# Performance work log

Measured on AMD Instinct MI355X. Metric: run time of the kernel, lower is better.

## Reference

```python
import jax, jax.numpy as jnp
import numpy as np

N, E, D, H, G = 100000, 1600000, 128, 256, 64
N0, N1 = 50000, 25000
SLOPE = 0.01  # PyTorch LeakyReLU default


def lrelu(x):
    return jax.nn.leaky_relu(x, SLOPE)


def seg_sum(x, idx, n):
    return jax.ops.segment_sum(x, idx, num_segments=n)


def seg_max(x, idx, n):
    m = jax.ops.segment_max(x, idx, num_segments=n)
    return jnp.where(jnp.isneginf(m), jnp.zeros_like(m), m)


def mpnn(x, edge_index, edge_attr, w1, b1, g, be, w2, b2):
    # MPNN.forward: add_self_loops -> node MLP -> sym-normalized, edge-weighted scatter-add
    n = x.shape[0]
    ar = jnp.arange(n)
    row = jnp.concatenate([edge_index[0], ar])  # source j (x_j gathered here)
    col = jnp.concatenate([edge_index[1], ar])  # target i (aggregation index)
    ea = jnp.concatenate([edge_attr, jnp.ones((n,), x.dtype)])  # self-loop fill=1.0
    # Linear -> BatchNorm1d(eval: mean0/var1) -> Dropout(eval: id) -> LeakyReLU -> Linear
    h = lrelu((x @ w1.T + b1) * g + be) @ w2.T + b2
    deg = seg_sum(jnp.ones(row.shape, x.dtype), row, n)
    dis = jnp.where(deg > 0, deg ** -0.5, 0.0)
    norm = dis[row] * dis[col]
    msg = (norm * ea)[:, None] * h[row]  # gather + elementwise weighting
    return seg_sum(msg, col, n)          # scatter-add aggregation


def _forward(x, edge_attr, energy, params, edge_index, batch, cluster0, cluster1):
    (w0a, b0a, g0, be0, w0b, b0b,
     w1a, b1a, g1, be1, w1b, b1b,
     w2a, b2a, g2, be2, w2b, b2b,
     emb_w, emb_b, emb_g, emb_be,
     lw1, lb1, lg, lbe, lw2, lb2) = params
    h = mpnn(x, edge_index, edge_attr, w0a, b0a, g0, be0, w0b, b0b) + x
    # --- first graclus max_pool (cluster0 precomputed; edges mapped w/o coalesce) ---
    px = seg_max(lrelu(h), cluster0, N0)
    ox = seg_max(x, cluster0, N0)  # max_pool(origin)
    pe = cluster0[edge_index]
    pb = jnp.maximum(jax.ops.segment_max(batch, cluster0, num_segments=N0), 0)
    # NOTE: mpnn_1 output is assigned to a local `x` and discarded in the original forward,
    # so it does not affect the result; we skip the dead computation.
    h2 = px + ox
    # --- second graclus max_pool ---
    px2 = seg_max(lrelu(h2), cluster1, N1)
    pe2 = cluster1[pe]
    pb2 = jnp.maximum(jax.ops.segment_max(pb, cluster1, num_segments=N1), 0)
    h3 = lrelu(mpnn(px2, pe2, edge_attr, w2a, b2a, g2, be2, w2b, b2b))
    gx = seg_max(h3, pb2, G)  # global_max_pool
    e = lrelu((energy.reshape(G, 21) @ emb_w.T + emb_b) * emb_g + emb_be)
    z = jnp.concatenate([gx, e], axis=1)  # [G, D+8]
    z = lrelu((z @ lw1.T + lb1) * lg + lbe)
    return z @ lw2.T + lb2  # [G, 1]


def setup_inputs() -> dict:
    key = jax.random.key(0)
    ks = iter(jax.random.split(key, 40))

    def lin(k, fo, fi):  # kaiming_normal_ fan_in, leaky_relu
        return jax.random.normal(k, (fo, fi), jnp.float32) * np.float32(np.sqrt(2.0 / fi))

    def bias(n):
        return jnp.full((n,), 0.01, jnp.float32)

    inp = {}
    inp['x'] = jax.random.normal(next(ks), (N, D), jnp.float32)
    inp['edge_attr'] = jax.random.uniform(next(ks), (E,), jnp.float32)
    inp['energy'] = jax.random.normal(next(ks), (G * 21,), jnp.float32)
    # mpnn_0 (D->D->D)
    inp['w0a'] = lin(next(ks), D, D); inp['b0a'] = bias(D)
    inp['g0'] = jnp.ones((D,), jnp.float32); inp['be0'] = jnp.zeros((D,), jnp.float32)
    inp['w0b'] = lin(next(ks), D, D); inp['b0b'] = bias(D)
    # mpnn_1 (D->D->D)  (dead in forward, kept as params)
    inp['w1a'] = lin(next(ks), D, D); inp['b1a'] = bias(D)
    inp['g1'] = jnp.ones((D,), jnp.float32); inp['be1'] = jnp.zeros((D,), jnp.float32)
    inp['w1b'] = lin(next(ks), D, D); inp['b1b'] = bias(D)
    # mpnn_2 (D->H->D)
    inp['w2a'] = lin(next(ks), H, D); inp['b2a'] = bias(H)
    inp['g2'] = jnp.ones((H,), jnp.float32); inp['be2'] = jnp.zeros((H,), jnp.float32)
    inp['w2b'] = lin(next(ks), D, H); inp['b2b'] = bias(D)
    # emb (21->8)
    inp['emb_w'] = lin(next(ks), 8, 21); inp['emb_b'] = bias(8)
    inp['emb_g'] = jnp.ones((8,), jnp.float32); inp['emb_be'] = jnp.zeros((8,), jnp.float32)
    # head ((D+8)->D->1)
    inp['lw1'] = lin(next(ks), D, D + 8); inp['lb1'] = bias(D)
    inp['lg'] = jnp.ones((D,), jnp.float32); inp['lbe'] = jnp.zeros((D,), jnp.float32)
    inp['lw2'] = lin(next(ks), 1, D); inp['lb2'] = bias(1)
    # int inputs
    inp['edge_index'] = jax.random.randint(next(ks), (2, E), 0, N, dtype=jnp.int32)
    inp['batch'] = jnp.sort(jax.random.randint(next(ks), (N,), 0, G, dtype=jnp.int32))
    inp['cluster0'] = jax.random.randint(next(ks), (N,), 0, N0, dtype=jnp.int32)
    inp['cluster1'] = jax.random.randint(next(ks), (N0,), 0, N1, dtype=jnp.int32)
    return inp


def reference(x, edge_attr, energy,
              w0a, b0a, g0, be0, w0b, b0b,
              w1a, b1a, g1, be1, w1b, b1b,
              w2a, b2a, g2, be2, w2b, b2b,
              emb_w, emb_b, emb_g, emb_be,
              lw1, lb1, lg, lbe, lw2, lb2,
              edge_index, batch, cluster0, cluster1):
    params = (w0a, b0a, g0, be0, w0b, b0b,
              w1a, b1a, g1, be1, w1b, b1b,
              w2a, b2a, g2, be2, w2b, b2b,
              emb_w, emb_b, emb_g, emb_be,
              lw1, lb1, lg, lbe, lw2, lb2)
    return _forward(x, edge_attr, energy, params, edge_index, batch, cluster0, cluster1)
```

## Files before the change

kernel.cpp:

```cpp
#include <hip/hip_runtime.h>
#include <math.h>

#define N_NODES 100000
#define N_EDGES 1600000
#define DIM     128
#define NPOOL0  50000
#define NPOOL1  25000
#define NGRAPH  64

typedef __attribute__((ext_vector_type(8))) short short8;
typedef __attribute__((ext_vector_type(4))) float f32x4;

__device__ __forceinline__ float lrelu(float v) { return v > 0.f ? v : 0.01f * v; }

__device__ __forceinline__ unsigned short f2bf(float f) {
    unsigned u = __float_as_uint(f);
    unsigned r = u + 0x7FFFu + ((u >> 16) & 1u);
    return (unsigned short)(r >> 16);
}

__device__ __forceinline__ void atomicMaxF(float* addr, float val) {
    if (val >= 0.f) atomicMax((int*)addr, __float_as_int(val));
    else            atomicMin((unsigned int*)addr, __float_as_uint(val));
}

__global__ __launch_bounds__(256) void fill_f32(float* __restrict__ p, int n, float v) {
    int i = blockIdx.x * 256 + threadIdx.x;
    if (i < n) p[i] = v;
}
__global__ __launch_bounds__(256) void fill_i32(int* __restrict__ p, int n, int v) {
    int i = blockIdx.x * 256 + threadIdx.x;
    if (i < n) p[i] = v;
}
__global__ __launch_bounds__(256) void conv_bf16(const float* __restrict__ in, unsigned short* __restrict__ out, int n) {
    int i = blockIdx.x * 256 + threadIdx.x;
    if (i < n) out[i] = f2bf(in[i]);
}

template<int KIN, int HID, bool BF16IN>
__global__ __launch_bounds__(256) void mlp_mfma(
        const void* __restrict__ Xv, int R,
        const unsigned short* __restrict__ W1, const float* __restrict__ B1,
        const float* __restrict__ G1, const float* __restrict__ BE1,
        const unsigned short* __restrict__ W2, const float* __restrict__ B2,
        unsigned short* __restrict__ Y)
{
    constexpr int XS_S = KIN + 8;
    constexpr int TS_S = HID + 8;
    __shared__ unsigned short xs[64 * XS_S];
    __shared__ unsigned short ts[64 * TS_S];

    const int tid = threadIdx.x;
    const int r0 = blockIdx.x * 64;

    {
        const int row = tid >> 2;
        const int c0 = (tid & 3) * 32;
        const int gr = r0 + row;
        if (BF16IN) {
            const unsigned short* X = (const unsigned short*)Xv;
            #pragma unroll
            for (int q = 0; q < 4; ++q) {
                short8 v = short8{0,0,0,0,0,0,0,0};
                if (gr < R) v = *(const short8*)&X[(size_t)gr * KIN + c0 + q * 8];
                *(short8*)&xs[row * XS_S + c0 + q * 8] = v;
            }
        } else {
            const float* X = (const float*)Xv;
            #pragma unroll
            for (int q = 0; q < 4; ++q) {
                short8 v = short8{0,0,0,0,0,0,0,0};
                if (gr < R) {
                    float4 a = *(const float4*)&X[(size_t)gr * KIN + c0 + q * 8];
                    float4 b = *(const float4*)&X[(size_t)gr * KIN + c0 + q * 8 + 4];
                    v[0] = (short)f2bf(a.x); v[1] = (short)f2bf(a.y);
                    v[2] = (short)f2bf(a.z); v[3] = (short)f2bf(a.w);
                    v[4] = (short)f2bf(b.x); v[5] = (short)f2bf(b.y);
                    v[6] = (short)f2bf(b.z); v[7] = (short)f2bf(b.w);
                }
                *(short8*)&xs[row * XS_S + c0 + q * 8] = v;
            }
        }
    }
    __syncthreads();

    const int wv = tid >> 6;
    const int lane = tid & 63;
    const int lr = lane & 15;
    const int lq = lane >> 4;
    const int arow = wv * 16 + lr;

    constexpr int NCG1 = HID / 16;
    constexpr int NK1 = KIN / 32;
    f32x4 acc1[NCG1] = {};
    for (int kc = 0; kc < NK1; ++kc) {
        short8 a = *(short8*)&xs[arow * XS_S + kc * 32 + lq * 8];
        #pragma unroll
        for (int cg = 0; cg < NCG1; ++cg) {
            short8 b = *(const short8*)&W1[(size_t)(cg * 16 + lr) * KIN + kc * 32 + lq * 8];
            acc1[cg] = __builtin_amdgcn_mfma_f32_16x16x32_bf16(a, b, acc1[cg], 0, 0, 0);
        }
    }
    #pragma unroll
    for (int cg = 0; cg < NCG1; ++cg) {
        const int c = cg * 16 + lr;
        const float bb = B1[c], gg = G1[c], ee = BE1[c];
        #pragma unroll
        for (int q = 0; q < 4; ++q) {
            const int rr = wv * 16 + lq * 4 + q;
            float v = (acc1[cg][q] + bb) * gg + ee;
            ts[rr * TS_S + c] = f2bf(lrelu(v));
        }
    }

    constexpr int NK2 = HID / 32;
    f32x4 acc2[8] = {};
    for (int kc = 0; kc < NK2; ++kc) {
        short8 a = *(short8*)&ts[arow * TS_S + kc * 32 + lq * 8];
        #pragma unroll
        for (int cg = 0; cg < 8; ++cg) {
            short8 b = *(const short8*)&W2[(size_t)(cg * 16 + lr) * HID + kc * 32 + lq * 8];
            acc2[cg] = __builtin_amdgcn_mfma_f32_16x16x32_bf16(a, b, acc2[cg], 0, 0, 0);
        }
    }
    #pragma unroll
    for (int cg = 0; cg < 8; ++cg) {
        const int c = cg * 16 + lr;
        const float bb = B2[c];
        #pragma unroll
        for (int q = 0; q < 4; ++q) {
            const int gr = r0 + wv * 16 + lq * 4 + q;
            if (gr < R) Y[(size_t)gr * 128 + c] = f2bf(acc2[cg][q] + bb);
        }
    }
}

__global__ __launch_bounds__(256) void count0(const int* __restrict__ src, const int* __restrict__ dst,
                                              float* __restrict__ deg, int* __restrict__ cnt, int E) {
    int e = blockIdx.x * 256 + threadIdx.x;
    if (e < E) {
        atomicAdd(&deg[src[e]], 1.0f);
        atomicAdd(&cnt[dst[e]], 1);
    }
}
__global__ __launch_bounds__(256) void rsqrt_ip(float* __restrict__ p, int n) {
    int i = blockIdx.x * 256 + threadIdx.x;
    if (i < n) p[i] = rsqrtf(p[i]);
}
__global__ __launch_bounds__(256) void scan_blk(const int* __restrict__ cnt, int* __restrict__ offs,
                                                int* __restrict__ bsum, int n) {
    __shared__ int s[256];
    const int tid = threadIdx.x;
    const int i = blockIdx.x * 256 + tid;
    int v = (i < n) ? cnt[i] : 0;
    s[tid] = v;
    __syncthreads();
    #pragma unroll
    for (int d = 1; d < 256; d <<= 1) {
        int t = (tid >= d) ? s[tid - d] : 0;
        __syncthreads();
        s[tid] += t;
        __syncthreads();
    }
    if (i < n) offs[i] = s[tid] - v;
    if (tid == 255) bsum[blockIdx.x] = s[255];
}
__global__ __launch_bounds__(512) void scan_top(int* __restrict__ bsum, int nb) {
    __shared__ int s[512];
    const int tid = threadIdx.x;
    int v = (tid < nb) ? bsum[tid] : 0;
    s[tid] = v;
    __syncthreads();
    #pragma unroll
    for (int d = 1; d < 512; d <<= 1) {
        int t = (tid >= d) ? s[tid - d] : 0;
        __syncthreads();
        s[tid] += t;
        __syncthreads();
    }
    if (tid < nb) bsum[tid] = s[tid] - v;
}
__global__ __launch_bounds__(256) void scan_add(int* __restrict__ offs, const int* __restrict__ bsum,
                                                int* __restrict__ fill, int n) {
    int i = blockIdx.x * 256 + threadIdx.x;
    if (i < n) {
        int o = offs[i] + bsum[i >> 8];
        offs[i] = o;
        fill[i] = o;
    }
}
__global__ __launch_bounds__(256) void place_pack(const int* __restrict__ dst, const int* __restrict__ srcA,
                                                  const float* __restrict__ ea, const float* __restrict__ dis,
                                                  int* __restrict__ fill, int2* __restrict__ pack, int E) {
    int e = blockIdx.x * 256 + threadIdx.x;
    if (e < E) {
        int d = dst[e];
        int s = srcA[e];
        int pos = atomicAdd(&fill[d], 1);
        pack[pos] = make_int2(s, __float_as_int(dis[s] * ea[e]));
    }
}
__global__ __launch_bounds__(256) void edgemap(
        const int* __restrict__ ei0, const int* __restrict__ ei1,
        const int* __restrict__ c0, const int* __restrict__ c1,
        int* __restrict__ src2, int* __restrict__ dst2,
        float* __restrict__ deg2, int* __restrict__ cnt2, int E)
{
    int e = blockIdx.x * 256 + threadIdx.x;
    if (e < E) {
        int s = c1[c0[ei0[e]]];
        int d = c1[c0[ei1[e]]];
        src2[e] = s;
        dst2[e] = d;
        atomicAdd(&deg2[s], 1.0f);
        atomicAdd(&cnt2[d], 1);
    }
}
__global__ __launch_bounds__(256) void seg_count(const int* __restrict__ map, int* __restrict__ cnt, int n) {
    int i = blockIdx.x * 256 + threadIdx.x;
    if (i < n) atomicAdd(&cnt[map[i]], 1);
}
__global__ __launch_bounds__(256) void place_idx(const int* __restrict__ map, int* __restrict__ fill,
                                                 int* __restrict__ list, int n) {
    int i = blockIdx.x * 256 + threadIdx.x;
    if (i < n) {
        int pos = atomicAdd(&fill[map[i]], 1);
        list[pos] = i;
    }
}
__global__ __launch_bounds__(256) void segmax_i32(const int* __restrict__ map, const int* __restrict__ vals,
                                                  int* __restrict__ out, int n) {
    int i = blockIdx.x * 256 + threadIdx.x;
    if (i < n) atomicMax(&out[map[i]], vals[i]);
}

#define EDGE_ITER(K, A0, A1) {                                                  \
    int s_ = __builtin_amdgcn_readlane(pv.x, (K));                              \
    float w_ = __int_as_float(__builtin_amdgcn_readlane(pv.y, (K)));            \
    unsigned hv_ = hrows[(size_t)s_ * 64 + lane];                               \
    float c_ = w_ * di;                                                         \
    A0 += c_ * __uint_as_float(hv_ << 16);                                      \
    A1 += c_ * __uint_as_float(hv_ & 0xFFFF0000u); }

__global__ __launch_bounds__(256) void gather0(
        const unsigned short* __restrict__ h16, const float* __restrict__ x,
        const float* __restrict__ dis, const int* __restrict__ offs,
        const int* __restrict__ cnt, const int2* __restrict__ pack,
        unsigned* __restrict__ agg0)
{
    const int wid = (blockIdx.x * 256 + threadIdx.x) >> 6;
    if (wid >= N_NODES) return;
    const int lane = threadIdx.x & 63;
    const float di = dis[wid];
    const unsigned* hrows = (const unsigned*)h16;

    unsigned hself = hrows[(size_t)wid * 64 + lane];
    float a0 = di * di * __uint_as_float(hself << 16);
    float a1 = di * di * __uint_as_float(hself & 0xFFFF0000u);
    float b0 = 0.f, b1 = 0.f;

    const int base = offs[wid], n = cnt[wid];
    int k0 = 0;
    for (; k0 + 64 <= n; k0 += 64) {
        int2 pv = pack[base + k0 + lane];
        #pragma unroll
        for (int k = 0; k < 64; k += 2) {
            EDGE_ITER(k,     a0, a1);
            EDGE_ITER(k + 1, b0, b1);
        }
    }
    const int rem = n - k0;
    if (rem > 0) {
        int2 pv = (lane < rem) ? pack[base + k0 + lane] : make_int2(0, 0);
        #pragma unroll 4
        for (int k = 0; k < rem; ++k) EDGE_ITER(k, a0, a1);
    }
    a0 += b0; a1 += b1;

    float2 xv = *(const float2*)&x[(size_t)wid * DIM + lane * 2];
    agg0[(size_t)wid * 64 + lane] =
        ((unsigned)f2bf(a1 + xv.y) << 16) | (unsigned)f2bf(a0 + xv.x);
}

__global__ __launch_bounds__(256) void gather2(
        const unsigned short* __restrict__ hm2,
        const float* __restrict__ dis, const int* __restrict__ offs,
        const int* __restrict__ cnt, const int2* __restrict__ pack,
        float* __restrict__ agg2)
{
    const int wid = (blockIdx.x * 256 + threadIdx.x) >> 6;
    if (wid >= NPOOL1) return;
    const int lane = threadIdx.x & 63;
    const float di = dis[wid];
    const unsigned* hrows = (const unsigned*)hm2;

    unsigned hself = hrows[(size_t)wid * 64 + lane];
    float a0 = di * di * __uint_as_float(hself << 16);
    float a1 = di * di * __uint_as_float(hself & 0xFFFF0000u);
    float b0 = 0.f, b1 = 0.f;

    const int base = offs[wid], n = cnt[wid];
    int k0 = 0;
    for (; k0 + 64 <= n; k0 += 64) {
        int2 pv = pack[base + k0 + lane];
        #pragma unroll
        for (int k = 0; k < 64; k += 2) {
            EDGE_ITER(k,     a0, a1);
            EDGE_ITER(k + 1, b0, b1);
        }
    }
    const int rem = n - k0;
    if (rem > 0) {
        int2 pv = (lane < rem) ? pack[base + k0 + lane] : make_int2(0, 0);
        #pragma unroll 4
        for (int k = 0; k < rem; ++k) EDGE_ITER(k, a0, a1);
    }
    a0 += b0; a1 += b1;

    float2 o = make_float2(lrelu(a0), lrelu(a1));
    *(float2*)&agg2[(size_t)wid * DIM + lane * 2] = o;
}

__global__ __launch_bounds__(256) void pool1_gather(
        const unsigned* __restrict__ agg0, const float* __restrict__ x,
        const int* __restrict__ offsc, const int* __restrict__ cntc,
        const int* __restrict__ listc, unsigned* __restrict__ h2)
{
    const int c = (blockIdx.x * 256 + threadIdx.x) >> 6;
    if (c >= NPOOL0) return;
    const int lane = threadIdx.x & 63;
    const int base = offsc[c], n = cntc[c];
    float p0 = -INFINITY, p1 = -INFINITY, o0 = -INFINITY, o1 = -INFINITY;
    for (int k = 0; k < n; ++k) {
        const int node = listc[base + k];
        const unsigned hv = agg0[(size_t)node * 64 + lane];
        const float2 xv = *(const float2*)&x[(size_t)node * 128 + lane * 2];
        p0 = fmaxf(p0, lrelu(__uint_as_float(hv << 16)));
        p1 = fmaxf(p1, lrelu(__uint_as_float(hv & 0xFFFF0000u)));
        o0 = fmaxf(o0, xv.x);
        o1 = fmaxf(o1, xv.y);
    }
    p0 = (p0 == -INFINITY) ? 0.f : p0;
    p1 = (p1 == -INFINITY) ? 0.f : p1;
    o0 = (o0 == -INFINITY) ? 0.f : o0;
    o1 = (o1 == -INFINITY) ? 0.f : o1;
    h2[(size_t)c * 64 + lane] =
        ((unsigned)f2bf(p1 + o1) << 16) | (unsigned)f2bf(p0 + o0);
}

__global__ __launch_bounds__(256) void pool2_gather(
        const unsigned* __restrict__ h2,
        const int* __restrict__ offsd, const int* __restrict__ cntd,
        const int* __restrict__ listd, unsigned* __restrict__ x2)
{
    const int d = (blockIdx.x * 256 + threadIdx.x) >> 6;
    if (d >= NPOOL1) return;
    const int lane = threadIdx.x & 63;
    const int base = offsd[d], n = cntd[d];
    float m0 = -INFINITY, m1 = -INFINITY;
    for (int k = 0; k < n; ++k) {
        const int node = listd[base + k];
        const unsigned hv = h2[(size_t)node * 64 + lane];
        m0 = fmaxf(m0, lrelu(__uint_as_float(hv << 16)));
        m1 = fmaxf(m1, lrelu(__uint_as_float(hv & 0xFFFF0000u)));
    }
    m0 = (m0 == -INFINITY) ? 0.f : m0;
    m1 = (m1 == -INFINITY) ? 0.f : m1;
    x2[(size_t)d * 64 + lane] = ((unsigned)f2bf(m1) << 16) | (unsigned)f2bf(m0);
}

__global__ __launch_bounds__(256) void gpool_scan(
        const float* __restrict__ agg2, const int* __restrict__ listg,
        const int* __restrict__ pb2, float* __restrict__ gmax)
{
    const int wave = (blockIdx.x * 256 + threadIdx.x) >> 6;
    const int lane = threadIdx.x & 63;
    const int CH = (NPOOL1 + 511) / 512;
    const int p0 = wave * CH;
    const int p1 = min(p0 + CH, NPOOL1);
    if (p0 >= NPOOL1) return;

    float m0 = -INFINITY, m1 = -INFINITY;
    int cur = -1;
    for (int p = p0; p < p1; ++p) {
        const int node = listg[p];
        const int g = pb2[node];
        if (g != cur) {
            if (cur >= 0) {
                float* gp = &gmax[(size_t)cur * DIM + lane * 2];
                atomicMaxF(gp + 0, m0);
                atomicMaxF(gp + 1, m1);
            }
            cur = g; m0 = -INFINITY; m1 = -INFINITY;
        }
        const float2 v = *(const float2*)&agg2[(size_t)node * DIM + lane * 2];
        m0 = fmaxf(m0, v.x);
        m1 = fmaxf(m1, v.y);
    }
    float* gp = &gmax[(size_t)cur * DIM + lane * 2];
    atomicMaxF(gp + 0, m0);
    atomicMaxF(gp + 1, m1);
}

__global__ __launch_bounds__(128) void head(
        const float* __restrict__ gmax, const float* __restrict__ energy,
        const float* __restrict__ emb_w, const float* __restrict__ emb_b,
        const float* __restrict__ emb_g, const float* __restrict__ emb_be,
        const float* __restrict__ lw1, const float* __restrict__ lb1,
        const float* __restrict__ lg, const float* __restrict__ lbe,
        const float* __restrict__ lw2, const float* __restrict__ lb2,
        float* __restrict__ out)
{
    const int g = blockIdx.x;
    const int t = threadIdx.x;
    __shared__ float z[136];
    __shared__ float red[128];

    {
        float v = gmax[(size_t)g * DIM + t];
        z[t] = (v == -INFINITY) ? 0.f : v;
    }
    if (t < 8) {
        float s = 0.f;
        #pragma unroll
        for (int k = 0; k < 21; ++k) s += energy[g * 21 + k] * emb_w[t * 21 + k];
        s = (s + emb_b[t]) * emb_g[t] + emb_be[t];
        z[128 + t] = lrelu(s);
    }
    __syncthreads();
    float s = 0.f;
    #pragma unroll 8
    for (int k = 0; k < 136; ++k) s += z[k] * lw1[t * 136 + k];
    float z2 = lrelu((s + lb1[t]) * lg[t] + lbe[t]);
    red[t] = z2 * lw2[t];
    __syncthreads();
    if (t == 0) {
        float acc = lb2[0];
        for (int k = 0; k < 128; ++k) acc += red[k];
        out[g] = acc;
    }
}

extern "C" void kernel_launch(void* const* d_in, const int* in_sizes, int n_in,
                              void* d_out, int out_size, void* d_ws, size_t ws_size,
                              hipStream_t stream) {
    const float* x        = (const float*)d_in[0];
    const float* edge_attr= (const float*)d_in[1];
    const float* energy   = (const float*)d_in[2];
    const float* w0a = (const float*)d_in[3];
    const float* b0a = (const float*)d_in[4];
    const float* g0  = (const float*)d_in[5];
    const float* be0 = (const float*)d_in[6];
    const float* w0b = (const float*)d_in[7];
    const float* b0b = (const float*)d_in[8];
    const float* w2a = (const float*)d_in[15];
    const float* b2a = (const float*)d_in[16];
    const float* g2  = (const float*)d_in[17];
    const float* be2 = (const float*)d_in[18];
    const float* w2b = (const float*)d_in[19];
    const float* b2b = (const float*)d_in[20];
    const float* emb_w  = (const float*)d_in[21];
    const float* emb_b  = (const float*)d_in[22];
    const float* emb_g  = (const float*)d_in[23];
    const float* emb_be = (const float*)d_in[24];
    const float* lw1 = (const float*)d_in[25];
    const float* lb1 = (const float*)d_in[26];
    const float* lg  = (const float*)d_in[27];
    const float* lbe = (const float*)d_in[28];
    const float* lw2 = (const float*)d_in[29];
    const float* lb2 = (const float*)d_in[30];
    const int* ei0   = (const int*)d_in[31];
    const int* ei1   = ei0 + N_EDGES;
    const int* batch = (const int*)d_in[32];
    const int* c0    = (const int*)d_in[33];
    const int* c1    = (const int*)d_in[34];
    float* out = (float*)d_out;

    char* ws = (char*)d_ws;
    unsigned short* h16 = (unsigned short*)(ws + 0);
    int*   src2  = (int*)(ws + 0);
    int*   dst2  = (int*)(ws + 6400000);
    float* agg2  = (float*)(ws + 12800000);
    unsigned* agg0 = (unsigned*)(ws + 25600000);
    unsigned short* hm2 = (unsigned short*)(ws + 25600000);
    int2*  pack0 = (int2*)(ws + 51200000);
    int2*  pack2 = (int2*)(ws + 51200000);
    unsigned* h2 = (unsigned*)(ws + 64000000);
    unsigned* x2 = (unsigned*)(ws + 76800000);
    float* deg0  = (float*)(ws + 83200000);
    int*   cnt0  = (int*)(ws + 83600000);
    int*   offs0 = (int*)(ws + 84000000);
    int*   fill0 = (int*)(ws + 84400000);
    int*   cntc  = (int*)(ws + 84800000);
    int*   offsc = (int*)(ws + 85000000);
    int*   fillc = (int*)(ws + 85200000);
    int*   listc = (int*)(ws + 85400000);
    int*   pb    = (int*)(ws + 85800000);
    int*   pb2   = (int*)(ws + 86000000);
    int*   cntd  = (int*)(ws + 86100000);
    int*   offsd = (int*)(ws + 86200000);
    int*   filld = (int*)(ws + 86300000);
    int*   listd = (int*)(ws + 86400000);
    float* deg2  = (float*)(ws + 86600000);
    int*   cnt2  = (int*)(ws + 86700000);
    int*   offs2 = (int*)(ws + 86800000);
    int*   fill2 = (int*)(ws + 86900000);
    int*   cntg  = (int*)(ws + 87000000);
    int*   offsg = (int*)(ws + 87000256);
    int*   fillg = (int*)(ws + 87000512);
    int*   listg = (int*)(ws + 87001088);
    int*   bsum  = (int*)(ws + 87102096);
    unsigned short* w0a16 = (unsigned short*)(ws + 87105000);
    unsigned short* w0b16 = (unsigned short*)(ws + 87138000);
    unsigned short* w2a16 = (unsigned short*)(ws + 87171000);
    unsigned short* w2b16 = (unsigned short*)(ws + 87237000);
    float* gmax  = (float*)(ws + 87303000);

    (void)in_sizes; (void)n_in; (void)out_size; (void)ws_size;

    const int NB0 = (N_NODES + 255) / 256;
    const int NBC = (NPOOL0 + 255) / 256;
    const int NB1 = (NPOOL1 + 255) / 256;
    const int NBE = (N_EDGES + 255) / 256;

    conv_bf16<<<64, 256, 0, stream>>>(w0a, w0a16, 16384);
    conv_bf16<<<64, 256, 0, stream>>>(w0b, w0b16, 16384);
    conv_bf16<<<128, 256, 0, stream>>>(w2a, w2a16, 32768);
    conv_bf16<<<128, 256, 0, stream>>>(w2b, w2b16, 32768);

    fill_f32<<<NB0, 256, 0, stream>>>(deg0, N_NODES, 1.0f);
    fill_i32<<<NB0, 256, 0, stream>>>(cnt0, N_NODES, 0);
    mlp_mfma<128, 128, false><<<(N_NODES + 63) / 64, 256, 0, stream>>>(
        x, N_NODES, w0a16, b0a, g0, be0, w0b16, b0b, h16);
    count0<<<NBE, 256, 0, stream>>>(ei0, ei1, deg0, cnt0, N_EDGES);
    rsqrt_ip<<<NB0, 256, 0, stream>>>(deg0, N_NODES);
    scan_blk<<<NB0, 256, 0, stream>>>(cnt0, offs0, bsum, N_NODES);
    scan_top<<<1, 512, 0, stream>>>(bsum, NB0);
    scan_add<<<NB0, 256, 0, stream>>>(offs0, bsum, fill0, N_NODES);
    place_pack<<<NBE, 256, 0, stream>>>(ei1, ei0, edge_attr, deg0, fill0, pack0, N_EDGES);
    gather0<<<(N_NODES * 64) / 256, 256, 0, stream>>>(h16, x, deg0, offs0, cnt0, pack0, agg0);

    fill_i32<<<NBC, 256, 0, stream>>>(cntc, NPOOL0, 0);
    seg_count<<<NB0, 256, 0, stream>>>(c0, cntc, N_NODES);
    scan_blk<<<NBC, 256, 0, stream>>>(cntc, offsc, bsum, NPOOL0);
    scan_top<<<1, 512, 0, stream>>>(bsum, NBC);
    scan_add<<<NBC, 256, 0, stream>>>(offsc, bsum, fillc, NPOOL0);
    place_idx<<<NB0, 256, 0, stream>>>(c0, fillc, listc, N_NODES);
    fill_i32<<<NBC, 256, 0, stream>>>(pb, NPOOL0, 0);
    segmax_i32<<<NB0, 256, 0, stream>>>(c0, batch, pb, N_NODES);
    pool1_gather<<<(NPOOL0 * 64) / 256, 256, 0, stream>>>(agg0, x, offsc, cntc, listc, h2);

    fill_i32<<<NB1, 256, 0, stream>>>(cntd, NPOOL1, 0);
    seg_count<<<NBC, 256, 0, stream>>>(c1, cntd, NPOOL0);
    scan_blk<<<NB1, 256, 0, stream>>>(cntd, offsd, bsum, NPOOL1);
    scan_top<<<1, 512, 0, stream>>>(bsum, NB1);
    scan_add<<<NB1, 256, 0, stream>>>(offsd, bsum, filld, NPOOL1);
    place_idx<<<NBC, 256, 0, stream>>>(c1, filld, listd, NPOOL0);
    fill_i32<<<NB1, 256, 0, stream>>>(pb2, NPOOL1, 0);
    segmax_i32<<<NBC, 256, 0, stream>>>(c1, pb, pb2, NPOOL0);
    pool2_gather<<<(NPOOL1 * 64) / 256, 256, 0, stream>>>(h2, offsd, cntd, listd, x2);

    fill_f32<<<NB1, 256, 0, stream>>>(deg2, NPOOL1, 1.0f);
    fill_i32<<<NB1, 256, 0, stream>>>(cnt2, NPOOL1, 0);
    edgemap<<<NBE, 256, 0, stream>>>(ei0, ei1, c0, c1, src2, dst2, deg2, cnt2, N_EDGES);
    rsqrt_ip<<<NB1, 256, 0, stream>>>(deg2, NPOOL1);
    scan_blk<<<NB1, 256, 0, stream>>>(cnt2, offs2, bsum, NPOOL1);
    scan_top<<<1, 512, 0, stream>>>(bsum, NB1);
    scan_add<<<NB1, 256, 0, stream>>>(offs2, bsum, fill2, NPOOL1);
    mlp_mfma<128, 256, true><<<(NPOOL1 + 63) / 64, 256, 0, stream>>>(
        x2, NPOOL1, w2a16, b2a, g2, be2, w2b16, b2b, hm2);
    place_pack<<<NBE, 256, 0, stream>>>(dst2, src2, edge_attr, deg2, fill2, pack2, N_EDGES);
    gather2<<<(NPOOL1 * 64) / 256, 256, 0, stream>>>(hm2, deg2, offs2, cnt2, pack2, agg2);

    fill_i32<<<1, 256, 0, stream>>>(cntg, NGRAPH, 0);
    seg_count<<<NB1, 256, 0, stream>>>(pb2, cntg, NPOOL1);
    scan_blk<<<1, 256, 0, stream>>>(cntg, offsg, bsum, NGRAPH);
    scan_top<<<1, 512, 0, stream>>>(bsum, 1);
    scan_add<<<1, 256, 0, stream>>>(offsg, bsum, fillg, NGRAPH);
    place_idx<<<NB1, 256, 0, stream>>>(pb2, fillg, listg, NPOOL1);
    fill_f32<<<(NGRAPH * DIM + 255) / 256, 256, 0, stream>>>(gmax, NGRAPH * DIM, -INFINITY);
    gpool_scan<<<128, 256, 0, stream>>>(agg2, listg, pb2, gmax);
    head<<<NGRAPH, 128, 0, stream>>>(gmax, energy, emb_w, emb_b, emb_g, emb_be,
                                     lw1, lb1, lg, lbe, lw2, lb2, out);
}
```

Baseline: 1.219 ms.

## Derive pooled-graph degrees from node degrees and batch init kernels

```diff
diff --git a/kernel.cpp b/kernel.cpp
--- a/kernel.cpp
+++ b/kernel.cpp
@@ -24,17 +24,23 @@
     else            atomicMin((unsigned int*)addr, __float_as_uint(val));
 }
 
-__global__ __launch_bounds__(256) void fill_f32(float* __restrict__ p, int n, float v) {
-    int i = blockIdx.x * 256 + threadIdx.x;
-    if (i < n) p[i] = v;
-}
-__global__ __launch_bounds__(256) void fill_i32(int* __restrict__ p, int n, int v) {
-    int i = blockIdx.x * 256 + threadIdx.x;
-    if (i < n) p[i] = v;
-}
-__global__ __launch_bounds__(256) void conv_bf16(const float* __restrict__ in, unsigned short* __restrict__ out, int n) {
-    int i = blockIdx.x * 256 + threadIdx.x;
-    if (i < n) out[i] = f2bf(in[i]);
+__global__ __launch_bounds__(256) void init_f(float* __restrict__ deg0, float* __restrict__ deg2,
+                                              float* __restrict__ gmax) {
+    int i = blockIdx.x * 256 + threadIdx.x;
+    if (i < N_NODES) deg0[i] = 1.0f;
+    else if (i < N_NODES + NPOOL1) deg2[i - N_NODES] = 1.0f;
+    else if (i < N_NODES + NPOOL1 + NGRAPH * DIM) gmax[i - N_NODES - NPOOL1] = -INFINITY;
+}
+__global__ __launch_bounds__(256) void conv_weights(
+        const float* __restrict__ w0a, const float* __restrict__ w0b,
+        const float* __restrict__ w2a, const float* __restrict__ w2b,
+        unsigned short* __restrict__ o0a, unsigned short* __restrict__ o0b,
+        unsigned short* __restrict__ o2a, unsigned short* __restrict__ o2b) {
+    int i = blockIdx.x * 256 + threadIdx.x;
+    if (i < 16384) o0a[i] = f2bf(w0a[i]);
+    else if (i < 32768) o0b[i - 16384] = f2bf(w0b[i - 16384]);
+    else if (i < 65536) o2a[i - 32768] = f2bf(w2a[i - 32768]);
+    else if (i < 98304) o2b[i - 65536] = f2bf(w2b[i - 65536]);
 }
 
 template<int KIN, int HID, bool BF16IN>
@@ -147,6 +153,20 @@
     int i = blockIdx.x * 256 + threadIdx.x;
     if (i < n) p[i] = rsqrtf(p[i]);
 }
+__global__ __launch_bounds__(256) void mapnode(
+        const int* __restrict__ c0, const int* __restrict__ c1,
+        const float* __restrict__ deg0, const int* __restrict__ cnt0,
+        int* __restrict__ cmap, float* __restrict__ deg2, int* __restrict__ cnt2, int n) {
+    int i = blockIdx.x * 256 + threadIdx.x;
+    if (i < n) {
+        int m = c1[c0[i]];
+        cmap[i] = m;
+        float oc = deg0[i] - 1.0f;
+        if (oc != 0.f) atomicAdd(&deg2[m], oc);
+        int ic = cnt0[i];
+        if (ic) atomicAdd(&cnt2[m], ic);
+    }
+}
 __global__ __launch_bounds__(256) void scan_blk(const int* __restrict__ cnt, int* __restrict__ offs,
                                                 int* __restrict__ bsum, int n) {
     __shared__ int s[256];
@@ -202,18 +222,13 @@
 }
 __global__ __launch_bounds__(256) void edgemap(
         const int* __restrict__ ei0, const int* __restrict__ ei1,
-        const int* __restrict__ c0, const int* __restrict__ c1,
-        int* __restrict__ src2, int* __restrict__ dst2,
-        float* __restrict__ deg2, int* __restrict__ cnt2, int E)
+        const int* __restrict__ cmap,
+        int* __restrict__ src2, int* __restrict__ dst2, int E)
 {
     int e = blockIdx.x * 256 + threadIdx.x;
     if (e < E) {
-        int s = c1[c0[ei0[e]]];
-        int d = c1[c0[ei1[e]]];
-        src2[e] = s;
-        dst2[e] = d;
-        atomicAdd(&deg2[s], 1.0f);
-        atomicAdd(&cnt2[d], 1);
+        src2[e] = cmap[ei0[e]];
+        dst2[e] = cmap[ei1[e]];
     }
 }
 __global__ __launch_bounds__(256) void seg_count(const int* __restrict__ map, int* __restrict__ cnt, int n) {
@@ -488,33 +503,36 @@
     unsigned* h2 = (unsigned*)(ws + 64000000);
     unsigned* x2 = (unsigned*)(ws + 76800000);
     float* deg0  = (float*)(ws + 83200000);
-    int*   cnt0  = (int*)(ws + 83600000);
-    int*   offs0 = (int*)(ws + 84000000);
-    int*   fill0 = (int*)(ws + 84400000);
-    int*   cntc  = (int*)(ws + 84800000);
-    int*   offsc = (int*)(ws + 85000000);
-    int*   fillc = (int*)(ws + 85200000);
-    int*   listc = (int*)(ws + 85400000);
-    int*   pb    = (int*)(ws + 85800000);
-    int*   pb2   = (int*)(ws + 86000000);
-    int*   cntd  = (int*)(ws + 86100000);
-    int*   offsd = (int*)(ws + 86200000);
-    int*   filld = (int*)(ws + 86300000);
-    int*   listd = (int*)(ws + 86400000);
-    float* deg2  = (float*)(ws + 86600000);
-    int*   cnt2  = (int*)(ws + 86700000);
-    int*   offs2 = (int*)(ws + 86800000);
-    int*   fill2 = (int*)(ws + 86900000);
-    int*   cntg  = (int*)(ws + 87000000);
+    float* deg2  = (float*)(ws + 83600000);
+    char*  zbase = ws + 83700000;
+    int*   cnt0  = (int*)(ws + 83700000);
+    int*   cnt2  = (int*)(ws + 84100000);
+    int*   cntc  = (int*)(ws + 84200000);
+    int*   cntd  = (int*)(ws + 84400000);
+    int*   cntg  = (int*)(ws + 84500000);
+    int*   pb    = (int*)(ws + 84500256);
+    int*   pb2   = (int*)(ws + 84700256);
+    const size_t ZBYTES = 84800256 - 83700000;
+    int*   offs0 = (int*)(ws + 84800256);
+    int*   fill0 = (int*)(ws + 85200256);
+    int*   offsc = (int*)(ws + 85600256);
+    int*   fillc = (int*)(ws + 85800256);
+    int*   listc = (int*)(ws + 86000256);
+    int*   offsd = (int*)(ws + 86400256);
+    int*   filld = (int*)(ws + 86500256);
+    int*   listd = (int*)(ws + 86600256);
+    int*   offs2 = (int*)(ws + 86800256);
+    int*   fill2 = (int*)(ws + 86900256);
     int*   offsg = (int*)(ws + 87000256);
     int*   fillg = (int*)(ws + 87000512);
-    int*   listg = (int*)(ws + 87001088);
-    int*   bsum  = (int*)(ws + 87102096);
-    unsigned short* w0a16 = (unsigned short*)(ws + 87105000);
-    unsigned short* w0b16 = (unsigned short*)(ws + 87138000);
-    unsigned short* w2a16 = (unsigned short*)(ws + 87171000);
-    unsigned short* w2b16 = (unsigned short*)(ws + 87237000);
-    float* gmax  = (float*)(ws + 87303000);
+    int*   listg = (int*)(ws + 87000768);
+    int*   bsum  = (int*)(ws + 87100768);
+    int*   cmap  = (int*)(ws + 87103000);
+    unsigned short* w0a16 = (unsigned short*)(ws + 87503000);
+    unsigned short* w0b16 = (unsigned short*)(ws + 87535768);
+    unsigned short* w2a16 = (unsigned short*)(ws + 87568536);
+    unsigned short* w2b16 = (unsigned short*)(ws + 87634072);
+    float* gmax  = (float*)(ws + 87699608);
 
     (void)in_sizes; (void)n_in; (void)out_size; (void)ws_size;
 
@@ -523,16 +541,14 @@
     const int NB1 = (NPOOL1 + 255) / 256;
     const int NBE = (N_EDGES + 255) / 256;
 
-    conv_bf16<<<64, 256, 0, stream>>>(w0a, w0a16, 16384);
-    conv_bf16<<<64, 256, 0, stream>>>(w0b, w0b16, 16384);
-    conv_bf16<<<128, 256, 0, stream>>>(w2a, w2a16, 32768);
-    conv_bf16<<<128, 256, 0, stream>>>(w2b, w2b16, 32768);
-
-    fill_f32<<<NB0, 256, 0, stream>>>(deg0, N_NODES, 1.0f);
-    fill_i32<<<NB0, 256, 0, stream>>>(cnt0, N_NODES, 0);
+    hipMemsetAsync(zbase, 0, ZBYTES, stream);
+    init_f<<<(N_NODES + NPOOL1 + NGRAPH * DIM + 255) / 256, 256, 0, stream>>>(deg0, deg2, gmax);
+    conv_weights<<<384, 256, 0, stream>>>(w0a, w0b, w2a, w2b, w0a16, w0b16, w2a16, w2b16);
+
     mlp_mfma<128, 128, false><<<(N_NODES + 63) / 64, 256, 0, stream>>>(
         x, N_NODES, w0a16, b0a, g0, be0, w0b16, b0b, h16);
     count0<<<NBE, 256, 0, stream>>>(ei0, ei1, deg0, cnt0, N_EDGES);
+    mapnode<<<NB0, 256, 0, stream>>>(c0, c1, deg0, cnt0, cmap, deg2, cnt2, N_NODES);
     rsqrt_ip<<<NB0, 256, 0, stream>>>(deg0, N_NODES);
     scan_blk<<<NB0, 256, 0, stream>>>(cnt0, offs0, bsum, N_NODES);
     scan_top<<<1, 512, 0, stream>>>(bsum, NB0);
@@ -540,29 +556,23 @@
     place_pack<<<NBE, 256, 0, stream>>>(ei1, ei0, edge_attr, deg0, fill0, pack0, N_EDGES);
     gather0<<<(N_NODES * 64) / 256, 256, 0, stream>>>(h16, x, deg0, offs0, cnt0, pack0, agg0);
 
-    fill_i32<<<NBC, 256, 0, stream>>>(cntc, NPOOL0, 0);
     seg_count<<<NB0, 256, 0, stream>>>(c0, cntc, N_NODES);
     scan_blk<<<NBC, 256, 0, stream>>>(cntc, offsc, bsum, NPOOL0);
     scan_top<<<1, 512, 0, stream>>>(bsum, NBC);
     scan_add<<<NBC, 256, 0, stream>>>(offsc, bsum, fillc, NPOOL0);
     place_idx<<<NB0, 256, 0, stream>>>(c0, fillc, listc, N_NODES);
-    fill_i32<<<NBC, 256, 0, stream>>>(pb, NPOOL0, 0);
     segmax_i32<<<NB0, 256, 0, stream>>>(c0, batch, pb, N_NODES);
     pool1_gather<<<(NPOOL0 * 64) / 256, 256, 0, stream>>>(agg0, x, offsc, cntc, listc, h2);
 
-    fill_i32<<<NB1, 256, 0, stream>>>(cntd, NPOOL1, 0);
     seg_count<<<NBC, 256, 0, stream>>>(c1, cntd, NPOOL0);
     scan_blk<<<NB1, 256, 0, stream>>>(cntd, offsd, bsum, NPOOL1);
     scan_top<<<1, 512, 0, stream>>>(bsum, NB1);
     scan_add<<<NB1, 256, 0, stream>>>(offsd, bsum, filld, NPOOL1);
     place_idx<<<NBC, 256, 0, stream>>>(c1, filld, listd, NPOOL0);
-    fill_i32<<<NB1, 256, 0, stream>>>(pb2, NPOOL1, 0);
     segmax_i32<<<NBC, 256, 0, stream>>>(c1, pb, pb2, NPOOL0);
     pool2_gather<<<(NPOOL1 * 64) / 256, 256, 0, stream>>>(h2, offsd, cntd, listd, x2);
 
-    fill_f32<<<NB1, 256, 0, stream>>>(deg2, NPOOL1, 1.0f);
-    fill_i32<<<NB1, 256, 0, stream>>>(cnt2, NPOOL1, 0);
-    edgemap<<<NBE, 256, 0, stream>>>(ei0, ei1, c0, c1, src2, dst2, deg2, cnt2, N_EDGES);
+    edgemap<<<NBE, 256, 0, stream>>>(ei0, ei1, cmap, src2, dst2, N_EDGES);
     rsqrt_ip<<<NB1, 256, 0, stream>>>(deg2, NPOOL1);
     scan_blk<<<NB1, 256, 0, stream>>>(cnt2, offs2, bsum, NPOOL1);
     scan_top<<<1, 512, 0, stream>>>(bsum, NB1);
@@ -572,13 +582,11 @@
     place_pack<<<NBE, 256, 0, stream>>>(dst2, src2, edge_attr, deg2, fill2, pack2, N_EDGES);
     gather2<<<(NPOOL1 * 64) / 256, 256, 0, stream>>>(hm2, deg2, offs2, cnt2, pack2, agg2);
 
-    fill_i32<<<1, 256, 0, stream>>>(cntg, NGRAPH, 0);
     seg_count<<<NB1, 256, 0, stream>>>(pb2, cntg, NPOOL1);
     scan_blk<<<1, 256, 0, stream>>>(cntg, offsg, bsum, NGRAPH);
     scan_top<<<1, 512, 0, stream>>>(bsum, 1);
     scan_add<<<1, 256, 0, stream>>>(offsg, bsum, fillg, NGRAPH);
     place_idx<<<NB1, 256, 0, stream>>>(pb2, fillg, listg, NPOOL1);
-    fill_f32<<<(NGRAPH * DIM + 255) / 256, 256, 0, stream>>>(gmax, NGRAPH * DIM, -INFINITY);
     gpool_scan<<<128, 256, 0, stream>>>(agg2, listg, pb2, gmax);
     head<<<NGRAPH, 128, 0, stream>>>(gmax, energy, emb_w, emb_b, emb_g, emb_be,
                                      lw1, lb1, lg, lbe, lw2, lb2, out);
```

Result: faster. 1.071 ms (-12.1%).
